# Kernel optimization log

Hardware: AMD Instinct MI355X
Metric: run time of the kernel (lower is better)

## Reference

```python
import jax, jax.numpy as jnp
import numpy as np
import math

B, S, D, H = 2, 2048, 1024, 16
DH = D // H  # dim_per_head = 64


def setup_inputs() -> dict:
    key = jax.random.key(0)
    ks = jax.random.split(key, 12)
    s = 1.0 / math.sqrt(D)
    return {
        "key": jax.random.normal(ks[0], (B, S, D), jnp.float32),
        "value": jax.random.normal(ks[1], (B, S, D), jnp.float32),
        "query": jax.random.normal(ks[2], (B, S, D), jnp.float32),
        "mask": jax.random.randint(ks[3], (B, S, S), 0, 2).astype(bool),
        "Wq": jax.random.normal(ks[4], (D, D), jnp.float32) * s,
        "bq": jnp.zeros((D,), jnp.float32),
        "Wk": jax.random.normal(ks[5], (D, D), jnp.float32) * s,
        "bk": jnp.zeros((D,), jnp.float32),
        "Wv": jax.random.normal(ks[6], (D, D), jnp.float32) * s,
        "bv": jnp.zeros((D,), jnp.float32),
        "Wo": jax.random.normal(ks[7], (D, D), jnp.float32) * s,
        "bo": jnp.zeros((D,), jnp.float32),
    }


def _shape(x):
    # [B, S, D] -> [B, H, S, DH]
    return x.reshape(B, -1, H, DH).transpose(0, 2, 1, 3)


def reference(key, value, query, mask, Wq, bq, Wk, bk, Wv, bv, Wo, bo):
    q = _shape(query @ Wq.T + bq)  # [B,H,Sq,DH]
    k = _shape(key @ Wk.T + bk)    # [B,H,Sk,DH]
    v = _shape(value @ Wv.T + bv)  # [B,H,Sk,DH]
    q = q / jnp.sqrt(jnp.asarray(DH, q.dtype))
    scores = jnp.einsum("bhqd,bhkd->bhqk", q, k)
    scores = jnp.where(mask[:, None, :, :], jnp.asarray(-1e18, scores.dtype), scores)
    attn = jax.nn.softmax(scores, axis=-1)
    # dropout is identity in eval/deterministic reference
    ctx = jnp.einsum("bhqk,bhkd->bhqd", attn, v)
    ctx = ctx.transpose(0, 2, 1, 3).reshape(B, -1, D)  # unshape
    return ctx @ Wo.T + bo
```

## Files before the change

### kernel.cpp

```cpp
#include <hip/hip_runtime.h>
#include <math.h>


constexpr int Bc  = 2;
constexpr int Sc  = 2048;
constexpr int Dc  = 1024;
constexpr int Hc  = 16;
constexpr int DHc = 64;
constexpr int BSc = Bc * Sc;

constexpr float LOG2E = 1.4426950408889634f;

typedef __bf16 bf16x8 __attribute__((ext_vector_type(8)));
typedef __bf16 bf16x4 __attribute__((ext_vector_type(4)));
typedef __bf16 bf16x2 __attribute__((ext_vector_type(2)));
typedef float  f32x4  __attribute__((ext_vector_type(4)));
typedef float  f32x16 __attribute__((ext_vector_type(16)));
typedef unsigned uint32x2 __attribute__((ext_vector_type(2)));
typedef unsigned uint32x4 __attribute__((ext_vector_type(4)));

#define GLDS16(gp, lp) __builtin_amdgcn_global_load_lds( \
    (const __attribute__((address_space(1))) void*)(gp), \
    (__attribute__((address_space(3))) void*)(lp), 16, 0, 0)

__global__ __launch_bounds__(256)
void wsplit(const float* __restrict__ W0, const float* __restrict__ W1,
            const float* __restrict__ W2, const float* __restrict__ W3,
            __bf16* __restrict__ out, __bf16* __restrict__ out2)
{
    const float* src[4] = {W0, W1, W2, W3};
    const int z = blockIdx.y;
    const size_t idx = ((size_t)blockIdx.x * 256 + threadIdx.x) * 4;
    const float4 v = *(const float4*)&src[z][idx];
    if (z == 3) {
        bf16x8 o;
        o[0] = (__bf16)v.x; o[1] = (__bf16)v.x;
        o[2] = (__bf16)v.y; o[3] = (__bf16)v.y;
        o[4] = (__bf16)v.z; o[5] = (__bf16)v.z;
        o[6] = (__bf16)v.w; o[7] = (__bf16)v.w;
        *(bf16x8*)&out2[idx * 2] = o;
    } else {
        bf16x4 o;
        o[0] = (__bf16)v.x; o[1] = (__bf16)v.y; o[2] = (__bf16)v.z; o[3] = (__bf16)v.w;
        *(bf16x4*)&out[(size_t)z * Dc * Dc + idx] = o;
    }
}

__global__ __launch_bounds__(256)
void acast(const float* __restrict__ A0, const float* __restrict__ A1,
           const float* __restrict__ A2, __bf16* __restrict__ out)
{
    const float* src[3] = {A0, A1, A2};
    const int z = blockIdx.y;
    const size_t idx = ((size_t)blockIdx.x * 256 + threadIdx.x) * 8;
    const float4 a = *(const float4*)&src[z][idx];
    const float4 b = *(const float4*)&src[z][idx + 4];
    bf16x8 o;
    o[0] = (__bf16)a.x; o[1] = (__bf16)a.y; o[2] = (__bf16)a.z; o[3] = (__bf16)a.w;
    o[4] = (__bf16)b.x; o[5] = (__bf16)b.y; o[6] = (__bf16)b.z; o[7] = (__bf16)b.w;
    *(bf16x8*)&out[(size_t)z * BSc * Dc + idx] = o;
}

template<int KD>
__device__ __forceinline__ void sweep128bb(const __bf16* __restrict__ A,
                                           const __bf16* __restrict__ Wh,
                                           char* AsB, char* WsB,
                                           int gm0, int gn0, f32x4 acc[4][4])
{
    const int tid  = threadIdx.x;
    const int w    = tid >> 6;
    const int lane = tid & 63;
    const int cc   = lane & 15;
    const int g    = lane >> 4;
    const int wm   = (w & 1) * 64;
    const int wn   = (w >> 1) * 64;

    int wrow[4], wchk[4];
#pragma unroll
    for (int r = 0; r < 4; ++r) {
        const int L = r * 256 + tid;
        wrow[r] = L >> 3;
        wchk[r] = (L & 7) ^ (wrow[r] & 7);
    }

#pragma unroll
    for (int r = 0; r < 4; ++r) {
        GLDS16(Wh + (size_t)(gn0 + wrow[r]) * KD + wchk[r] * 8,
               WsB + (r * 256 + tid) * 16);
        GLDS16(A + (size_t)(gm0 + wrow[r]) * KD + wchk[r] * 8,
               AsB + (r * 256 + tid) * 16);
    }

    for (int it = 0; it < KD / 64; ++it) {
        const char* As = AsB + (it & 1) * 16384;
        const char* Ws = WsB + (it & 1) * 16384;
        __syncthreads();

        if (it + 1 < KD / 64) {
            const int kn = (it + 1) * 64;
            char* Wn = WsB + ((it + 1) & 1) * 16384;
            char* An = AsB + ((it + 1) & 1) * 16384;
#pragma unroll
            for (int r = 0; r < 4; ++r) {
                GLDS16(Wh + (size_t)(gn0 + wrow[r]) * KD + kn + wchk[r] * 8,
                       Wn + (r * 256 + tid) * 16);
                GLDS16(A + (size_t)(gm0 + wrow[r]) * KD + kn + wchk[r] * 8,
                       An + (r * 256 + tid) * 16);
            }
        }

        __builtin_amdgcn_s_setprio(1);
#pragma unroll
        for (int kk = 0; kk < 2; ++kk) {
            const int cb4 = (kk * 4 + g) << 4;
            bf16x8 af[4], bfr[4];
#pragma unroll
            for (int mt = 0; mt < 4; ++mt) {
                const int row = wm + mt * 16 + cc;
                af[mt] = *(const bf16x8*)(As + row * 128 + (cb4 ^ ((row & 7) << 4)));
            }
#pragma unroll
            for (int nt = 0; nt < 4; ++nt) {
                const int row = wn + nt * 16 + cc;
                bfr[nt] = *(const bf16x8*)(Ws + row * 128 + (cb4 ^ ((row & 7) << 4)));
            }
#pragma unroll
            for (int mt = 0; mt < 4; ++mt)
#pragma unroll
                for (int nt = 0; nt < 4; ++nt)
                    acc[mt][nt] = __builtin_amdgcn_mfma_f32_16x16x32_bf16(
                        af[mt], bfr[nt], acc[mt][nt], 0, 0, 0);
        }
        __builtin_amdgcn_s_setprio(0);
    }
}

template<int KD>
__device__ __forceinline__ void sweep64bb(const __bf16* __restrict__ A,
                                          const __bf16* __restrict__ Wh,
                                          char* AsB, char* WsB,
                                          int gm0, int gn0, f32x4 acc[2][4])
{
    const int tid  = threadIdx.x;
    const int w    = tid >> 6;
    const int lane = tid & 63;
    const int cc   = lane & 15;
    const int g    = lane >> 4;
    const int wm   = (w & 1) * 32;
    const int wn   = (w >> 1) * 64;

    int wrow[4], wchk[4];
#pragma unroll
    for (int r = 0; r < 4; ++r) {
        const int L = r * 256 + tid;
        wrow[r] = L >> 3;
        wchk[r] = (L & 7) ^ (wrow[r] & 7);
    }
    int arow[2], achk[2];
#pragma unroll
    for (int r = 0; r < 2; ++r) {
        const int L = r * 256 + tid;
        arow[r] = L >> 3;
        achk[r] = (L & 7) ^ (arow[r] & 7);
    }

#pragma unroll
    for (int r = 0; r < 4; ++r)
        GLDS16(Wh + (size_t)(gn0 + wrow[r]) * KD + wchk[r] * 8,
               WsB + (r * 256 + tid) * 16);
#pragma unroll
    for (int r = 0; r < 2; ++r)
        GLDS16(A + (size_t)(gm0 + arow[r]) * KD + achk[r] * 8,
               AsB + (r * 256 + tid) * 16);

    for (int it = 0; it < KD / 64; ++it) {
        const char* As = AsB + (it & 1) * 8192;
        const char* Ws = WsB + (it & 1) * 16384;
        __syncthreads();

        if (it + 1 < KD / 64) {
            const int kn = (it + 1) * 64;
            char* Wn = WsB + ((it + 1) & 1) * 16384;
            char* An = AsB + ((it + 1) & 1) * 8192;
#pragma unroll
            for (int r = 0; r < 4; ++r)
                GLDS16(Wh + (size_t)(gn0 + wrow[r]) * KD + kn + wchk[r] * 8,
                       Wn + (r * 256 + tid) * 16);
#pragma unroll
            for (int r = 0; r < 2; ++r)
                GLDS16(A + (size_t)(gm0 + arow[r]) * KD + kn + achk[r] * 8,
                       An + (r * 256 + tid) * 16);
        }

        __builtin_amdgcn_s_setprio(1);
#pragma unroll
        for (int kk = 0; kk < 2; ++kk) {
            const int cb4 = (kk * 4 + g) << 4;
            bf16x8 af[2], bfr[4];
#pragma unroll
            for (int mt = 0; mt < 2; ++mt) {
                const int row = wm + mt * 16 + cc;
                af[mt] = *(const bf16x8*)(As + row * 128 + (cb4 ^ ((row & 7) << 4)));
            }
#pragma unroll
            for (int nt = 0; nt < 4; ++nt) {
                const int row = wn + nt * 16 + cc;
                bfr[nt] = *(const bf16x8*)(Ws + row * 128 + (cb4 ^ ((row & 7) << 4)));
            }
#pragma unroll
            for (int mt = 0; mt < 2; ++mt)
#pragma unroll
                for (int nt = 0; nt < 4; ++nt)
                    acc[mt][nt] = __builtin_amdgcn_mfma_f32_16x16x32_bf16(
                        af[mt], bfr[nt], acc[mt][nt], 0, 0, 0);
        }
        __builtin_amdgcn_s_setprio(0);
    }
}

__global__ __launch_bounds__(256)
void qkv_mfma(const __bf16* __restrict__ Abf, const __bf16* __restrict__ Whi,
              const float* __restrict__ bq, const float* __restrict__ bk,
              const float* __restrict__ bv,
              __bf16* __restrict__ Qo, __bf16* __restrict__ Ko, __bf16* __restrict__ Vt)
{
    __shared__ __align__(16) char smem[65536];

    const int z = blockIdx.z;
    const float* bias = (z == 0) ? bq : (z == 1) ? bk : bv;
    const float scale = (z == 0) ? 0.125f * LOG2E : 1.0f;
    const __bf16* A   = Abf + (size_t)z * BSc * Dc;
    const __bf16* Wh  = Whi + (size_t)z * Dc * Dc;

    const int gm0 = blockIdx.x * 128;
    const int gn0 = blockIdx.y * 128;

    f32x4 acc[4][4];
#pragma unroll
    for (int mt = 0; mt < 4; ++mt)
#pragma unroll
        for (int nt = 0; nt < 4; ++nt) acc[mt][nt] = {0.f, 0.f, 0.f, 0.f};

    sweep128bb<Dc>(A, Wh, smem, smem + 32768, gm0, gn0, acc);

    const int tid = threadIdx.x;
    const int w = tid >> 6, lane = tid & 63;
    const int cc = lane & 15, g = lane >> 4;
    const int wm = (w & 1) * 64, wn = (w >> 1) * 64;

    float bias4[4];
#pragma unroll
    for (int nt = 0; nt < 4; ++nt) bias4[nt] = bias[gn0 + wn + nt * 16 + cc];

    if (z == 2) {
#pragma unroll
        for (int mt = 0; mt < 4; ++mt)
#pragma unroll
            for (int nt = 0; nt < 4; ++nt) {
                const int col = gn0 + wn + nt * 16 + cc;
                const int h = col >> 6, dh = col & 63;
                const int row0 = gm0 + wm + mt * 16 + g * 4;
                const int b = row0 >> 11, s0 = row0 & 2047;
                bf16x4 vv;
#pragma unroll
                for (int reg = 0; reg < 4; ++reg)
                    vv[reg] = (__bf16)(acc[mt][nt][reg] + bias4[nt]);
                *(bf16x4*)&Vt[(((size_t)(b * Hc + h)) * DHc + dh) * Sc + s0] = vv;
            }
    } else {
        __bf16* O = (z == 0) ? Qo : Ko;
#pragma unroll
        for (int mt = 0; mt < 4; ++mt)
#pragma unroll
            for (int nt = 0; nt < 4; ++nt) {
                const int col = gn0 + wn + nt * 16 + cc;
                const int h = col >> 6, dh = col & 63;
#pragma unroll
                for (int reg = 0; reg < 4; ++reg) {
                    const int row = gm0 + wm + mt * 16 + g * 4 + reg;
                    const int b = row >> 11, s = row & 2047;
                    O[(((size_t)(b * Hc + h)) * Sc + s) * DHc + dh] =
                        (__bf16)((acc[mt][nt][reg] + bias4[nt]) * scale);
                }
            }
    }
}

__global__ __launch_bounds__(256)
void out_mfma(const __bf16* __restrict__ ctx2, const __bf16* __restrict__ Wo2,
              const float* __restrict__ bo, float* __restrict__ out)
{
    __shared__ __align__(16) char smem[49152];

    const int gm0 = blockIdx.x * 64;
    const int gn0 = blockIdx.y * 128;

    f32x4 acc[2][4];
#pragma unroll
    for (int mt = 0; mt < 2; ++mt)
#pragma unroll
        for (int nt = 0; nt < 4; ++nt) acc[mt][nt] = {0.f, 0.f, 0.f, 0.f};

    sweep64bb<2 * Dc>(ctx2, Wo2, smem + 32768, smem, gm0, gn0, acc);

    const int tid = threadIdx.x;
    const int w = tid >> 6, lane = tid & 63;
    const int cc = lane & 15, g = lane >> 4;
    const int wm = (w & 1) * 32, wn = (w >> 1) * 64;

    float bias4[4];
#pragma unroll
    for (int nt = 0; nt < 4; ++nt) bias4[nt] = bo[gn0 + wn + nt * 16 + cc];

#pragma unroll
    for (int mt = 0; mt < 2; ++mt)
#pragma unroll
        for (int nt = 0; nt < 4; ++nt) {
            const int col = gn0 + wn + nt * 16 + cc;
#pragma unroll
            for (int reg = 0; reg < 4; ++reg) {
                const int row = gm0 + wm + mt * 16 + g * 4 + reg;
                out[(size_t)row * Dc + col] = acc[mt][nt][reg] + bias4[nt];
            }
        }
}

__global__ __launch_bounds__(256)
void mask_pack(const int* __restrict__ mask, unsigned long long* __restrict__ out)
{
    const int lane = threadIdx.x & 63;
    const size_t waveBase = ((size_t)blockIdx.x * 4 + (threadIdx.x >> 6)) * 256;
    unsigned long long b0 = __ballot(mask[waveBase + lane]        != 0);
    unsigned long long b1 = __ballot(mask[waveBase + 64 + lane]   != 0);
    unsigned long long b2 = __ballot(mask[waveBase + 128 + lane]  != 0);
    unsigned long long b3 = __ballot(mask[waveBase + 192 + lane]  != 0);
    if (lane == 0) {
        unsigned long long* dst = out + (waveBase >> 6);
        dst[0] = b0; dst[1] = b1; dst[2] = b2; dst[3] = b3;
    }
}

__global__ __launch_bounds__(256, 2)
void attn_mfma(const __bf16* __restrict__ Q, const __bf16* __restrict__ K,
               const __bf16* __restrict__ Vt,
               const unsigned long long* __restrict__ mp,
               __bf16* __restrict__ ctx2)
{
    __shared__ __align__(16) char smem[32768];

    const int tid  = threadIdx.x;
    const int w    = tid >> 6;
    const int lane = tid & 63;
    const int c    = lane & 31;
    const int u    = lane >> 5;
    const int bh   = blockIdx.y;
    const int b    = bh >> 4;
    const int h    = bh & 15;
    const int qw   = blockIdx.x * 128 + w * 32;

    const __bf16* Qb  = Q  + (size_t)bh * Sc * DHc;
    const __bf16* Kb  = K  + (size_t)bh * Sc * DHc;
    const __bf16* Vtb = Vt + (size_t)bh * DHc * Sc;

    bf16x8 qa[4];
#pragma unroll
    for (int ch = 0; ch < 4; ++ch)
        qa[ch] = *(const bf16x8*)&Qb[(size_t)(qw + c) * DHc + ch * 16 + u * 8];

    f32x16 o[2], o2[2];
#pragma unroll
    for (int dt = 0; dt < 2; ++dt)
#pragma unroll
        for (int i = 0; i < 16; ++i) { o[dt][i] = 0.f; o2[dt][i] = 0.f; }
    float lp[4] = {0.f, 0.f, 0.f, 0.f};

    const int ci[2] = {tid, 256 + tid};
    int rowi[2], ski[2];
#pragma unroll
    for (int i = 0; i < 2; ++i) {
        rowi[i] = ci[i] >> 3;
        ski[i]  = (ci[i] & 7) ^ (rowi[i] & 7);
    }

#pragma unroll
    for (int i = 0; i < 2; ++i) {
        GLDS16(Kb + (size_t)rowi[i] * DHc + ski[i] * 8,
               smem + ci[i] * 16);
        GLDS16(Vtb + (size_t)rowi[i] * Sc + ski[i] * 8,
               smem + 8192 + ci[i] * 16);
    }

    for (int it = 0; it < 32; ++it) {
        const char* Ks = smem + (it & 1) * 16384;
        const char* Vs = Ks + 8192;

        __syncthreads();

        if (it + 1 < 32) {
            char* Kn = smem + ((it + 1) & 1) * 16384;
            const int kn = (it + 1) * 64;
#pragma unroll
            for (int i = 0; i < 2; ++i) {
                GLDS16(Kb + (size_t)(kn + rowi[i]) * DHc + ski[i] * 8,
                       Kn + ci[i] * 16);
                GLDS16(Vtb + (size_t)rowi[i] * Sc + kn + ski[i] * 8,
                       Kn + 8192 + ci[i] * 16);
            }
        }

        const unsigned long long mw =
            mp[((size_t)(b * Sc + qw + c) << 5) + it];

        f32x16 sc[2];
        __builtin_amdgcn_s_setprio(1);
#pragma unroll
        for (int nt = 0; nt < 2; ++nt) {
            f32x16 z0, z1;
#pragma unroll
            for (int i = 0; i < 16; ++i) { z0[i] = -24.f; z1[i] = 0.f; }
            const int row = nt * 32 + c;
            const int rx  = (row & 7) << 4;
            const bf16x8 kb0 = *(const bf16x8*)(Ks + row * 128 + ((0  + u * 16) ^ rx));
            const bf16x8 kb1 = *(const bf16x8*)(Ks + row * 128 + ((32 + u * 16) ^ rx));
            const bf16x8 kb2 = *(const bf16x8*)(Ks + row * 128 + ((64 + u * 16) ^ rx));
            const bf16x8 kb3 = *(const bf16x8*)(Ks + row * 128 + ((96 + u * 16) ^ rx));
            z0 = __builtin_amdgcn_mfma_f32_32x32x16_bf16(kb0, qa[0], z0, 0, 0, 0);
            z1 = __builtin_amdgcn_mfma_f32_32x32x16_bf16(kb1, qa[1], z1, 0, 0, 0);
            z0 = __builtin_amdgcn_mfma_f32_32x32x16_bf16(kb2, qa[2], z0, 0, 0, 0);
            z1 = __builtin_amdgcn_mfma_f32_32x32x16_bf16(kb3, qa[3], z1, 0, 0, 0);
            sc[nt] = z0 + z1;
        }
        __builtin_amdgcn_s_setprio(0);

        unsigned pk[2][4][2];
#pragma unroll
        for (int nt = 0; nt < 2; ++nt)
#pragma unroll
            for (int rr = 0; rr < 4; ++rr) {
                const unsigned nib =
                    (unsigned)(mw >> (nt * 32 + rr * 8 + u * 4)) & 0xFu;
                float pv[4];
#pragma unroll
                for (int r = 0; r < 4; ++r) {
                    float p = __builtin_amdgcn_exp2f(sc[nt][rr * 4 + r]);
                    p = (nib & (1u << r)) ? 0.f : p;
                    lp[rr] += p;
                    pv[r] = p;
                }
                bf16x2 t0; t0[0] = (__bf16)pv[0]; t0[1] = (__bf16)pv[1];
                bf16x2 t1; t1[0] = (__bf16)pv[2]; t1[1] = (__bf16)pv[3];
                pk[nt][rr][0] = __builtin_bit_cast(unsigned, t0);
                pk[nt][rr][1] = __builtin_bit_cast(unsigned, t1);
            }

        bf16x8 pa[4];
#pragma unroll
        for (int kc = 0; kc < 4; ++kc) {
            const int nt = kc >> 1;
            const int r0 = (kc & 1) * 2;
            uint32x2 s0 = __builtin_amdgcn_permlane32_swap(
                pk[nt][r0][0], pk[nt][r0 + 1][0], false, false);
            uint32x2 s1 = __builtin_amdgcn_permlane32_swap(
                pk[nt][r0][1], pk[nt][r0 + 1][1], false, false);
            uint32x4 wds;
            wds[0] = s0[0]; wds[1] = s1[0]; wds[2] = s0[1]; wds[3] = s1[1];
            pa[kc] = __builtin_bit_cast(bf16x8, wds);
        }

        __builtin_amdgcn_s_setprio(1);
#pragma unroll
        for (int dt = 0; dt < 2; ++dt) {
            const int row = dt * 32 + c;
            const int rx  = (row & 7) << 4;
            const bf16x8 vb0 = *(const bf16x8*)(Vs + row * 128 + ((0  + u * 16) ^ rx));
            const bf16x8 vb1 = *(const bf16x8*)(Vs + row * 128 + ((32 + u * 16) ^ rx));
            const bf16x8 vb2 = *(const bf16x8*)(Vs + row * 128 + ((64 + u * 16) ^ rx));
            const bf16x8 vb3 = *(const bf16x8*)(Vs + row * 128 + ((96 + u * 16) ^ rx));
            o[dt]  = __builtin_amdgcn_mfma_f32_32x32x16_bf16(pa[0], vb0, o[dt],  0, 0, 0);
            o2[dt] = __builtin_amdgcn_mfma_f32_32x32x16_bf16(pa[1], vb1, o2[dt], 0, 0, 0);
            o[dt]  = __builtin_amdgcn_mfma_f32_32x32x16_bf16(pa[2], vb2, o[dt],  0, 0, 0);
            o2[dt] = __builtin_amdgcn_mfma_f32_32x32x16_bf16(pa[3], vb3, o2[dt], 0, 0, 0);
        }
        __builtin_amdgcn_s_setprio(0);
    }

    float lsum = (lp[0] + lp[1]) + (lp[2] + lp[3]);
    lsum += __shfl_xor(lsum, 32);
    const float linv = 1.0f / lsum;

    float inv[16];
#pragma unroll
    for (int i = 0; i < 16; ++i)
        inv[i] = __shfl(linv, (i & 3) + 8 * (i >> 2) + 4 * u);

#pragma unroll
    for (int dt = 0; dt < 2; ++dt)
#pragma unroll
        for (int i = 0; i < 16; ++i) {
            const int q = qw + (i & 3) + 8 * (i >> 2) + 4 * u;
            const int col = h * 64 + dt * 32 + c;
            const float v = (o[dt][i] + o2[dt][i]) * inv[i];
            const __bf16 hi = (__bf16)v;
            bf16x2 hv;
            hv[0] = hi;
            hv[1] = (__bf16)(v - (float)hi);
            *(bf16x2*)&ctx2[(((size_t)b * Sc + q) * Dc + col) * 2] = hv;
        }
}

extern "C" void kernel_launch(void* const* d_in, const int* in_sizes, int n_in,
                              void* d_out, int out_size, void* d_ws, size_t ws_size,
                              hipStream_t stream)
{
    const float* key   = (const float*)d_in[0];
    const float* value = (const float*)d_in[1];
    const float* query = (const float*)d_in[2];
    const int*   mask  = (const int*)  d_in[3];
    const float* Wq    = (const float*)d_in[4];
    const float* bq    = (const float*)d_in[5];
    const float* Wk    = (const float*)d_in[6];
    const float* bk    = (const float*)d_in[7];
    const float* Wv    = (const float*)d_in[8];
    const float* bv    = (const float*)d_in[9];
    const float* Wo    = (const float*)d_in[10];
    const float* bo    = (const float*)d_in[11];
    float* out = (float*)d_out;

    char* wsb = (char*)d_ws;
    __bf16* Qbf  = (__bf16*)(wsb);
    __bf16* Kbf  = (__bf16*)(wsb + ((size_t)8  << 20));
    __bf16* Vt   = (__bf16*)(wsb + ((size_t)16 << 20));
    unsigned long long* mpk = (unsigned long long*)(wsb + ((size_t)24 << 20));
    __bf16* Whi  = (__bf16*)(wsb + ((size_t)25 << 20));
    __bf16* Wo2  = (__bf16*)(wsb + ((size_t)31 << 20));
    __bf16* ctx2 = (__bf16*)(wsb + ((size_t)35 << 20));
    __bf16* Abf  = (__bf16*)(wsb + ((size_t)51 << 20));

    dim3 gws(Dc * Dc / (256 * 4), 4);
    wsplit<<<gws, 256, 0, stream>>>(Wq, Wk, Wv, Wo, Whi, Wo2);

    dim3 gac(BSc * Dc / (256 * 8), 3);
    acast<<<gac, 256, 0, stream>>>(query, key, value, Abf);

    dim3 gqkv(BSc / 128, Dc / 128, 3);
    qkv_mfma<<<gqkv, 256, 0, stream>>>(Abf, Whi, bq, bk, bv, Qbf, Kbf, Vt);

    const int mask_n = Bc * Sc * Sc;
    mask_pack<<<mask_n / 1024, 256, 0, stream>>>(mask, mpk);

    dim3 gattn(Sc / 128, Bc * Hc);
    attn_mfma<<<gattn, 256, 0, stream>>>(Qbf, Kbf, Vt, mpk, ctx2);

    dim3 gout(BSc / 64, Dc / 128);
    out_mfma<<<gout, 256, 0, stream>>>(ctx2, Wo2, bo, out);
}
```

Before: 267.4 us.

## Software-pipeline attention with triple-buffered K/V and swizzle out-proj block order

The attention kernel now uses three LDS stages and issues the QK^T MFMAs for the next tile before the softmax and PV work of the current tile, so exp and mask work can overlap with matrix ops. It also replaces the split dual accumulators with single accumulation chains. The output projection moves to a 1D grid with a remapped block order that groups tiles to improve L2 reuse. The cost is more LDS per block (48KB), which may limit occupancy, plus extra live score registers that add register pressure.

Result: no change. 263.6 us (-1.4%).

```diff
diff --git a/kernel.cpp b/kernel.cpp
--- a/kernel.cpp
+++ b/kernel.cpp
@@ -292,8 +292,9 @@
 {
     __shared__ __align__(16) char smem[49152];
 
-    const int gm0 = blockIdx.x * 64;
-    const int gn0 = blockIdx.y * 128;
+    const int lb = (blockIdx.x & 7) * 64 + (blockIdx.x >> 3);
+    const int gm0 = ((lb >> 6) * 8 + (lb & 7)) * 64;
+    const int gn0 = ((lb >> 3) & 7) * 128;
 
     f32x4 acc[2][4];
 #pragma unroll
@@ -340,13 +341,102 @@
     }
 }
 
+__device__ __forceinline__ void stage_kv(const __bf16* Kb, const __bf16* Vtb,
+                                         char* B, int kn,
+                                         int rowi0, int ski0, int ci0,
+                                         int rowi1, int ski1, int ci1)
+{
+    GLDS16(Kb + (size_t)(kn + rowi0) * DHc + ski0 * 8, B + ci0 * 16);
+    GLDS16(Vtb + (size_t)rowi0 * Sc + kn + ski0 * 8, B + 8192 + ci0 * 16);
+    GLDS16(Kb + (size_t)(kn + rowi1) * DHc + ski1 * 8, B + ci1 * 16);
+    GLDS16(Vtb + (size_t)rowi1 * Sc + kn + ski1 * 8, B + 8192 + ci1 * 16);
+}
+
+__device__ __forceinline__ void qk_tile(const char* Ks, const bf16x8 qa[4],
+                                        int c, int u, f32x16& s0, f32x16& s1)
+{
+    __builtin_amdgcn_s_setprio(1);
+#pragma unroll
+    for (int nt = 0; nt < 2; ++nt) {
+        f32x16 z;
+#pragma unroll
+        for (int i = 0; i < 16; ++i) z[i] = -24.f;
+        const int row = nt * 32 + c;
+        const int rx  = (row & 7) << 4;
+#pragma unroll
+        for (int ch = 0; ch < 4; ++ch) {
+            const bf16x8 kb = *(const bf16x8*)
+                (Ks + row * 128 + ((ch * 32 + u * 16) ^ rx));
+            z = __builtin_amdgcn_mfma_f32_32x32x16_bf16(kb, qa[ch], z, 0, 0, 0);
+        }
+        if (nt == 0) s0 = z; else s1 = z;
+    }
+    __builtin_amdgcn_s_setprio(0);
+}
+
+__device__ __forceinline__ void smpv_tile(const char* Vs,
+                                          const f32x16& s0, const f32x16& s1,
+                                          unsigned long long mw, int c, int u,
+                                          float lp[4], f32x16 o[2])
+{
+    unsigned pk[2][4][2];
+#pragma unroll
+    for (int nt = 0; nt < 2; ++nt)
+#pragma unroll
+        for (int rr = 0; rr < 4; ++rr) {
+            const unsigned nib =
+                (unsigned)(mw >> (nt * 32 + rr * 8 + u * 4)) & 0xFu;
+            float pv[4];
+#pragma unroll
+            for (int r = 0; r < 4; ++r) {
+                float p = __builtin_amdgcn_exp2f(
+                    (nt == 0) ? s0[rr * 4 + r] : s1[rr * 4 + r]);
+                p = (nib & (1u << r)) ? 0.f : p;
+                lp[rr] += p;
+                pv[r] = p;
+            }
+            bf16x2 t0; t0[0] = (__bf16)pv[0]; t0[1] = (__bf16)pv[1];
+            bf16x2 t1; t1[0] = (__bf16)pv[2]; t1[1] = (__bf16)pv[3];
+            pk[nt][rr][0] = __builtin_bit_cast(unsigned, t0);
+            pk[nt][rr][1] = __builtin_bit_cast(unsigned, t1);
+        }
+
+    bf16x8 pa[4];
+#pragma unroll
+    for (int kc = 0; kc < 4; ++kc) {
+        const int nt = kc >> 1;
+        const int r0 = (kc & 1) * 2;
+        uint32x2 w0 = __builtin_amdgcn_permlane32_swap(
+            pk[nt][r0][0], pk[nt][r0 + 1][0], false, false);
+        uint32x2 w1 = __builtin_amdgcn_permlane32_swap(
+            pk[nt][r0][1], pk[nt][r0 + 1][1], false, false);
+        uint32x4 wds;
+        wds[0] = w0[0]; wds[1] = w1[0]; wds[2] = w0[1]; wds[3] = w1[1];
+        pa[kc] = __builtin_bit_cast(bf16x8, wds);
+    }
+
+    __builtin_amdgcn_s_setprio(1);
+#pragma unroll
+    for (int dt = 0; dt < 2; ++dt) {
+        const int row = dt * 32 + c;
+        const int rx  = (row & 7) << 4;
+#pragma unroll
+        for (int kc = 0; kc < 4; ++kc) {
+            const bf16x8 vb = *(const bf16x8*)
+                (Vs + row * 128 + ((kc * 32 + u * 16) ^ rx));
+            o[dt] = __builtin_amdgcn_mfma_f32_32x32x16_bf16(pa[kc], vb, o[dt], 0, 0, 0);
+        }
+    }
+    __builtin_amdgcn_s_setprio(0);
+}
+
 __global__ __launch_bounds__(256, 2)
 void attn_mfma(const __bf16* __restrict__ Q, const __bf16* __restrict__ K,
                const __bf16* __restrict__ Vt,
                const unsigned long long* __restrict__ mp,
                __bf16* __restrict__ ctx2)
 {
-    __shared__ __align__(16) char smem[32768];
+    __shared__ __align__(16) char smem[49152];
 
     const int tid  = threadIdx.x;
     const int w    = tid >> 6;
@@ -367,121 +457,48 @@
     for (int ch = 0; ch < 4; ++ch)
         qa[ch] = *(const bf16x8*)&Qb[(size_t)(qw + c) * DHc + ch * 16 + u * 8];
 
-    f32x16 o[2], o2[2];
+    f32x16 o[2];
 #pragma unroll
     for (int dt = 0; dt < 2; ++dt)
 #pragma unroll
-        for (int i = 0; i < 16; ++i) { o[dt][i] = 0.f; o2[dt][i] = 0.f; }
+        for (int i = 0; i < 16; ++i) o[dt][i] = 0.f;
     float lp[4] = {0.f, 0.f, 0.f, 0.f};
 
-    const int ci[2] = {tid, 256 + tid};
-    int rowi[2], ski[2];
-#pragma unroll
-    for (int i = 0; i < 2; ++i) {
-        rowi[i] = ci[i] >> 3;
-        ski[i]  = (ci[i] & 7) ^ (rowi[i] & 7);
-    }
-
-#pragma unroll
-    for (int i = 0; i < 2; ++i) {
-        GLDS16(Kb + (size_t)rowi[i] * DHc + ski[i] * 8,
-               smem + ci[i] * 16);
-        GLDS16(Vtb + (size_t)rowi[i] * Sc + ski[i] * 8,
-               smem + 8192 + ci[i] * 16);
-    }
-
-    for (int it = 0; it < 32; ++it) {
-        const char* Ks = smem + (it & 1) * 16384;
-        const char* Vs = Ks + 8192;
-
+    const int ci0 = tid,        ci1 = 256 + tid;
+    const int rowi0 = ci0 >> 3, rowi1 = ci1 >> 3;
+    const int ski0 = (ci0 & 7) ^ (rowi0 & 7);
+    const int ski1 = (ci1 & 7) ^ (rowi1 & 7);
+
+    const size_t mbase = ((size_t)(b * Sc + qw + c) << 5);
+
+    stage_kv(Kb, Vtb, smem,         0,  rowi0, ski0, ci0, rowi1, ski1, ci1);
+    stage_kv(Kb, Vtb, smem + 16384, 64, rowi0, ski0, ci0, rowi1, ski1, ci1);
+    __syncthreads();
+
+    unsigned long long mwA = mp[mbase + 0], mwB;
+    f32x16 sA0, sA1, sB0, sB1;
+    qk_tile(smem, qa, c, u, sA0, sA1);
+
+    for (int tp = 0; tp < 16; ++tp) {
+        const int t0 = tp * 2;
         __syncthreads();
-
-        if (it + 1 < 32) {
-            char* Kn = smem + ((it + 1) & 1) * 16384;
-            const int kn = (it + 1) * 64;
-#pragma unroll
-            for (int i = 0; i < 2; ++i) {
-                GLDS16(Kb + (size_t)(kn + rowi[i]) * DHc + ski[i] * 8,
-                       Kn + ci[i] * 16);
-                GLDS16(Vtb + (size_t)rowi[i] * Sc + kn + ski[i] * 8,
-                       Kn + 8192 + ci[i] * 16);
-            }
-        }
-
-        const unsigned long long mw =
-            mp[((size_t)(b * Sc + qw + c) << 5) + it];
-
-        f32x16 sc[2];
-        __builtin_amdgcn_s_setprio(1);
-#pragma unroll
-        for (int nt = 0; nt < 2; ++nt) {
-            f32x16 z0, z1;
-#pragma unroll
-            for (int i = 0; i < 16; ++i) { z0[i] = -24.f; z1[i] = 0.f; }
-            const int row = nt * 32 + c;
-            const int rx  = (row & 7) << 4;
-            const bf16x8 kb0 = *(const bf16x8*)(Ks + row * 128 + ((0  + u * 16) ^ rx));
-            const bf16x8 kb1 = *(const bf16x8*)(Ks + row * 128 + ((32 + u * 16) ^ rx));
-            const bf16x8 kb2 = *(const bf16x8*)(Ks + row * 128 + ((64 + u * 16) ^ rx));
-            const bf16x8 kb3 = *(const bf16x8*)(Ks + row * 128 + ((96 + u * 16) ^ rx));
-            z0 = __builtin_amdgcn_mfma_f32_32x32x16_bf16(kb0, qa[0], z0, 0, 0, 0);
-            z1 = __builtin_amdgcn_mfma_f32_32x32x16_bf16(kb1, qa[1], z1, 0, 0, 0);
-            z0 = __builtin_amdgcn_mfma_f32_32x32x16_bf16(kb2, qa[2], z0, 0, 0, 0);
-            z1 = __builtin_amdgcn_mfma_f32_32x32x16_bf16(kb3, qa[3], z1, 0, 0, 0);
-            sc[nt] = z0 + z1;
-        }
-        __builtin_amdgcn_s_setprio(0);
-
-        unsigned pk[2][4][2];
-#pragma unroll
-        for (int nt = 0; nt < 2; ++nt)
-#pragma unroll
-            for (int rr = 0; rr < 4; ++rr) {
-                const unsigned nib =
-                    (unsigned)(mw >> (nt * 32 + rr * 8 + u * 4)) & 0xFu;
-                float pv[4];
-#pragma unroll
-                for (int r = 0; r < 4; ++r) {
-                    float p = __builtin_amdgcn_exp2f(sc[nt][rr * 4 + r]);
-                    p = (nib & (1u << r)) ? 0.f : p;
-                    lp[rr] += p;
-                    pv[r] = p;
-                }
-                bf16x2 t0; t0[0] = (__bf16)pv[0]; t0[1] = (__bf16)pv[1];
-                bf16x2 t1; t1[0] = (__bf16)pv[2]; t1[1] = (__bf16)pv[3];
-                pk[nt][rr][0] = __builtin_bit_cast(unsigned, t0);
-                pk[nt][rr][1] = __builtin_bit_cast(unsigned, t1);
-            }
-
-        bf16x8 pa[4];
-#pragma unroll
-        for (int kc = 0; kc < 4; ++kc) {
-            const int nt = kc >> 1;
-            const int r0 = (kc & 1) * 2;
-            uint32x2 s0 = __builtin_amdgcn_permlane32_swap(
-                pk[nt][r0][0], pk[nt][r0 + 1][0], false, false);
-            uint32x2 s1 = __builtin_amdgcn_permlane32_swap(
-                pk[nt][r0][1], pk[nt][r0 + 1][1], false, false);
-            uint32x4 wds;
-            wds[0] = s0[0]; wds[1] = s1[0]; wds[2] = s0[1]; wds[3] = s1[1];
-            pa[kc] = __builtin_bit_cast(bf16x8, wds);
-        }
-
-        __builtin_amdgcn_s_setprio(1);
-#pragma unroll
-        for (int dt = 0; dt < 2; ++dt) {
-            const int row = dt * 32 + c;
-            const int rx  = (row & 7) << 4;
-            const bf16x8 vb0 = *(const bf16x8*)(Vs + row * 128 + ((0  + u * 16) ^ rx));
-            const bf16x8 vb1 = *(const bf16x8*)(Vs + row * 128 + ((32 + u * 16) ^ rx));
-            const bf16x8 vb2 = *(const bf16x8*)(Vs + row * 128 + ((64 + u * 16) ^ rx));
-            const bf16x8 vb3 = *(const bf16x8*)(Vs + row * 128 + ((96 + u * 16) ^ rx));
-            o[dt]  = __builtin_amdgcn_mfma_f32_32x32x16_bf16(pa[0], vb0, o[dt],  0, 0, 0);
-            o2[dt] = __builtin_amdgcn_mfma_f32_32x32x16_bf16(pa[1], vb1, o2[dt], 0, 0, 0);
-            o[dt]  = __builtin_amdgcn_mfma_f32_32x32x16_bf16(pa[2], vb2, o[dt],  0, 0, 0);
-            o2[dt] = __builtin_amdgcn_mfma_f32_32x32x16_bf16(pa[3], vb3, o2[dt], 0, 0, 0);
-        }
-        __builtin_amdgcn_s_setprio(0);
+        if (t0 + 2 < 32)
+            stage_kv(Kb, Vtb, smem + ((t0 + 2) % 3) * 16384, (t0 + 2) * 64,
+                     rowi0, ski0, ci0, rowi1, ski1, ci1);
+        mwB = mp[mbase + (t0 + 1)];
+        qk_tile(smem + ((t0 + 1) % 3) * 16384, qa, c, u, sB0, sB1);
+        smpv_tile(smem + (t0 % 3) * 16384 + 8192, sA0, sA1, mwA, c, u, lp, o);
+
+        const int t1 = t0 + 1;
+        __syncthreads();
+        if (t1 + 2 < 32)
+            stage_kv(Kb, Vtb, smem + ((t1 + 2) % 3) * 16384, (t1 + 2) * 64,
+                     rowi0, ski0, ci0, rowi1, ski1, ci1);
+        if (t1 + 1 < 32) {
+            mwA = mp[mbase + (t1 + 1)];
+            qk_tile(smem + ((t1 + 1) % 3) * 16384, qa, c, u, sA0, sA1);
+        }
+        smpv_tile(smem + (t1 % 3) * 16384 + 8192, sB0, sB1, mwB, c, u, lp, o);
     }
 
     float lsum = (lp[0] + lp[1]) + (lp[2] + lp[3]);
@@ -499,7 +516,7 @@
         for (int i = 0; i < 16; ++i) {
             const int q = qw + (i & 3) + 8 * (i >> 2) + 4 * u;
             const int col = h * 64 + dt * 32 + c;
-            const float v = (o[dt][i] + o2[dt][i]) * inv[i];
+            const float v = o[dt][i] * inv[i];
             const __bf16 hi = (__bf16)v;
             bf16x2 hv;
             hv[0] = hi;
@@ -551,6 +568,5 @@
     dim3 gattn(Sc / 128, Bc * Hc);
     attn_mfma<<<gattn, 256, 0, stream>>>(Qbf, Kbf, Vt, mpk, ctx2);
 
-    dim3 gout(BSc / 64, Dc / 128);
-    out_mfma<<<gout, 256, 0, stream>>>(ctx2, Wo2, bo, out);
-}
+    out_mfma<<<dim3(512), 256, 0, stream>>>(ctx2, Wo2, bo, out);
+}
```
